# Kernel optimization log

Measured on AMD Instinct MI355X. Metric: run time of the kernel, lower is better.

Reference implementation:

```python
import jax, jax.numpy as jnp
import numpy as np

B, LQ, LKV = 2, 4096, 2048
DQ = DK = DV = 1024
H, DQK, DHV = 16, 64, 64
DOUT = 1024


def _band_mask(span, stride):
    # additive mask: 0 where 0 <= row - col*stride < span, else -inf
    rows = jnp.arange(LQ)[:, None]
    cols = jnp.arange(LKV)[None, :]
    s = rows - cols * stride
    valid = (s >= 0) & (s < span)
    return jnp.where(valid, 0.0, -jnp.inf).astype(jnp.float32)  # [LQ, LKV]


def setup_inputs() -> dict:
    key = jax.random.key(0)
    ks = jax.random.split(key, 7)
    return {
        "q": jax.random.normal(ks[0], (B, LQ, DQ), jnp.float32),
        "k": jax.random.normal(ks[1], (B, LKV, DK), jnp.float32),
        "v": jax.random.normal(ks[2], (B, LKV, DV), jnp.float32),
        # Linear weights stored as [in, out] (x @ W == torch Linear with W.T)
        "Wq": jax.random.normal(ks[3], (DQ, H * DQK), jnp.float32) / np.sqrt(DQ).astype(np.float32),
        "Wk": jax.random.normal(ks[4], (DK, H * DQK), jnp.float32) / np.sqrt(DK).astype(np.float32),
        "Wv": jax.random.normal(ks[5], (DV, H * DHV), jnp.float32) / np.sqrt(DV).astype(np.float32),
        "Wo": jax.random.normal(ks[6], (H * DHV, DOUT), jnp.float32) / np.sqrt(H * DHV).astype(np.float32),
        "span": 16,
        "stride": 2,
    }


def reference(q, k, v, Wq, Wk, Wv, Wo, span, stride):
    mask = _band_mask(span, stride)  # [LQ, LKV]
    Q = (q @ Wq).reshape(B, LQ, H, DQK)   # [B, LQ, H, DQK]
    K = (k @ Wk).reshape(B, LKV, H, DQK)  # [B, LKV, H, DQK]
    V = (v @ Wv).reshape(B, LKV, H, DHV)  # [B, LKV, H, DHV]
    scores = jnp.einsum("bqhd,bkhd->bhqk", Q, K) + mask  # [B, H, LQ, LKV]
    # NOTE: original code softmaxes over dim 2 == the QUERY axis (faithful)
    attn = jax.nn.softmax(scores, axis=2)
    ctx = jnp.einsum("bhqk,bkhd->bqhd", attn, V).reshape(B, LQ, H * DHV)
    return ctx @ Wo  # [B, LQ, DOUT]
```

## Files before the change

### kernel.cpp

```cpp
#include <hip/hip_runtime.h>
#include <cstdint>
#include <cstddef>


typedef _Float16 f16;
typedef _Float16 f16x8 __attribute__((ext_vector_type(8)));
typedef float v4f __attribute__((ext_vector_type(4)));

#define B_  2
#define LQ_ 4096
#define LKV_ 2048
#define DMODEL 1024
#define NH 16
#define HD 64
#define SPAN 16
#define STRIDE 2

#define NQ_ELEMS  ((size_t)B_ * LQ_ * DMODEL)
#define NKV_ELEMS ((size_t)B_ * LKV_ * DMODEL)

__device__ __forceinline__ void async_copy16(const f16* g, f16* l) {
    __builtin_amdgcn_global_load_lds((const __attribute__((address_space(1))) void*)g,
                                     (__attribute__((address_space(3))) void*)l, 16, 0, 0);
}

__global__ __launch_bounds__(256)
void prep_all(const float* __restrict__ W0, const float* __restrict__ W1,
              const float* __restrict__ W2, const float* __restrict__ W3,
              f16* __restrict__ T0, f16* __restrict__ T1,
              f16* __restrict__ T2, f16* __restrict__ T3,
              const float* __restrict__ q, const float* __restrict__ k,
              const float* __restrict__ v,
              f16* __restrict__ qh, f16* __restrict__ kh, f16* __restrict__ vh) {
    const int t = threadIdx.x;
    const int bid = blockIdx.x;
    if (bid < 1024) {
        const int z = bid >> 8, rem = bid & 255;
        const int bx = rem & 15, byy = rem >> 4;
        const float* W;
        f16* Wt;
        switch (z) {
            case 0: W = W0; Wt = T0; break;
            case 1: W = W1; Wt = T1; break;
            case 2: W = W2; Wt = T2; break;
            default: W = W3; Wt = T3; break;
        }
        __shared__ float tile[64][65];
        const int r0 = byy * 64, c0 = bx * 64;
        const int tx = t & 63, ty = t >> 6;
        for (int i = ty; i < 64; i += 4)
            tile[i][tx] = W[(long)(r0 + i) * DMODEL + c0 + tx];
        __syncthreads();
        for (int i = ty; i < 64; i += 4)
            Wt[(long)(c0 + i) * DMODEL + r0 + tx] = (f16)tile[tx][i];
    } else {
        const int cid = bid - 1024;
        const float* src;
        f16* dst;
        size_t base;
        if (cid < 4096)      { src = q; dst = qh; base = (size_t)cid * 2048; }
        else if (cid < 6144) { src = k; dst = kh; base = (size_t)(cid - 4096) * 2048; }
        else                 { src = v; dst = vh; base = (size_t)(cid - 6144) * 2048; }
        const size_t i = base + (size_t)t * 8;
        const float4 lo = *(const float4*)(src + i);
        const float4 hi = *(const float4*)(src + i + 4);
        f16x8 o = {(f16)lo.x, (f16)lo.y, (f16)lo.z, (f16)lo.w,
                   (f16)hi.x, (f16)hi.y, (f16)hi.z, (f16)hi.w};
        *(f16x8*)(dst + i) = o;
    }
}

template <bool OUT_F32>
__device__ __forceinline__ void gemm_body(const f16* __restrict__ Ah,
                                          const f16* __restrict__ Bt,
                                          void* __restrict__ Cv,
                                          int rowTile, int colTile) {
    constexpr int K = DMODEL, N = DMODEL;
    __shared__ f16 As[128 * 64];
    __shared__ f16 Bs[128 * 64];
    const int t = threadIdx.x;
    const int lane = t & 63;
    const int w = t >> 6;
    const int wm = w >> 1, wn = w & 1;
    const long rowBase = (long)rowTile * 128;
    const long colBase = (long)colTile * 128;
    const int qrow = lane & 15;
    const int quad = lane >> 4;

    v4f acc[4][4] = {};

    const int srow = t >> 3;
    const int schunk = t & 7;
    const int gchunk = schunk ^ (srow & 7);
    const f16* aptr = Ah + (rowBase + srow) * (long)K + gchunk * 8;
    const f16* bptr = Bt + (colBase + srow) * (long)K + gchunk * 8;
    f16* lA = &As[srow * 64 + schunk * 8];
    f16* lB = &Bs[srow * 64 + schunk * 8];

    for (int k0 = 0; k0 < K; k0 += 64) {
#pragma unroll
        for (int i = 0; i < 4; ++i)
            async_copy16(bptr + k0 + i * 32 * (long)K, lB + i * 2048);
#pragma unroll
        for (int i = 0; i < 4; ++i)
            async_copy16(aptr + k0 + i * 32 * (long)K, lA + i * 2048);
        __syncthreads();
#pragma unroll
        for (int s = 0; s < 2; ++s) {
            const int xk = (s * 4 + quad) ^ (qrow & 7);
            f16x8 af[4], bf[4];
#pragma unroll
            for (int mt = 0; mt < 4; ++mt)
                af[mt] = *(const f16x8*)(&As[(wm * 64 + mt * 16 + qrow) * 64 + xk * 8]);
#pragma unroll
            for (int nt = 0; nt < 4; ++nt)
                bf[nt] = *(const f16x8*)(&Bs[(wn * 64 + nt * 16 + qrow) * 64 + xk * 8]);
#pragma unroll
            for (int mt = 0; mt < 4; ++mt)
#pragma unroll
                for (int nt = 0; nt < 4; ++nt)
                    acc[mt][nt] = __builtin_amdgcn_mfma_f32_16x16x32_f16(
                        af[mt], bf[nt], acc[mt][nt], 0, 0, 0);
        }
        __syncthreads();
    }

#pragma unroll
    for (int mt = 0; mt < 4; ++mt)
#pragma unroll
        for (int nt = 0; nt < 4; ++nt) {
            const long col = colBase + wn * 64 + nt * 16 + qrow;
#pragma unroll
            for (int r = 0; r < 4; ++r) {
                const long row = rowBase + wm * 64 + mt * 16 + quad * 4 + r;
                if (OUT_F32)
                    ((float*)Cv)[row * (long)N + col] = acc[mt][nt][r];
                else
                    ((f16*)Cv)[row * (long)N + col] = (f16)acc[mt][nt][r];
            }
        }
}

__global__ __launch_bounds__(256, 2)
void gemm_qkv(const f16* __restrict__ A0, const f16* __restrict__ A1,
              const f16* __restrict__ A2, const f16* __restrict__ B0,
              const f16* __restrict__ B1, const f16* __restrict__ B2,
              f16* __restrict__ C0, f16* __restrict__ C1, f16* __restrict__ C2) {
    const int id = blockIdx.x;
    const int xcd = id & 7;
    const int g = id >> 3;
    const int ct = g & 7;
    int rowIdx = (g >> 3) + xcd * 16;
    const f16* A;
    const f16* Bt;
    f16* C;
    if (rowIdx < 64) {
        A = A0; Bt = B0; C = C0;
    } else if (rowIdx < 96) {
        A = A1; Bt = B1; C = C1; rowIdx -= 64;
    } else {
        A = A2; Bt = B2; C = C2; rowIdx -= 96;
    }
    gemm_body<false>(A, Bt, (void*)C, rowIdx, ct);
}

__global__ __launch_bounds__(256, 2)
void gemm_out(const f16* __restrict__ A, const f16* __restrict__ Bt,
              float* __restrict__ C) {
    const int id = blockIdx.x;
    const int xcd = id & 7;
    const int g = id >> 3;
    const int ct = g & 7;
    const int rowIdx = (g >> 3) + xcd * 8;
    gemm_body<true>(A, Bt, (void*)C, rowIdx, ct);
}

__global__ __launch_bounds__(256)
void attn_scores(const f16* __restrict__ Q, const f16* __restrict__ Km,
                 float* __restrict__ attnw) {
    const int c0 = blockIdx.x * 4, b = blockIdx.y;
    const int t = threadIdx.x;
    __shared__ f16 Qs[24 * 1032];
    __shared__ f16 Ks[4 * 1032];

#pragma unroll
    for (int it = 0; it < 12; ++it) {
        const int ch = t + 256 * it;
        const int row = ch >> 7, off = (ch & 127) * 8;
        int qq = 2 * c0 + row;
        if (qq > LQ_ - 1) qq = LQ_ - 1;
        f16x8 x = *(const f16x8*)(Q + (size_t)(b * LQ_ + qq) * DMODEL + off);
        const int h = off >> 6, bb = (off >> 3) & 7;
        *(f16x8*)(&Qs[row * 1032 + h * 64 + ((bb + h) & 7) * 8]) = x;
    }
#pragma unroll
    for (int it = 0; it < 2; ++it) {
        const int ch = t + 256 * it;
        const int row = ch >> 7, off = (ch & 127) * 8;
        f16x8 x = *(const f16x8*)(Km + (size_t)(b * LKV_ + c0 + row) * DMODEL + off);
        const int h = off >> 6, bb = (off >> 3) & 7;
        *(f16x8*)(&Ks[row * 1032 + h * 64 + ((bb + h) & 7) * 8]) = x;
    }
    __syncthreads();

    const int h = t >> 4, j = t & 15;
#pragma unroll
    for (int ci = 0; ci < 4; ++ci) {
        const int c = c0 + ci;
        const int q = STRIDE * c + j;
        const int row = 2 * ci + j;
        float a = 0.f;
#pragma unroll
        for (int bb = 0; bb < 8; ++bb) {
            const int off = h * 64 + ((bb + h) & 7) * 8;
            f16x8 qv = *(const f16x8*)(&Qs[row * 1032 + off]);
            f16x8 kv = *(const f16x8*)(&Ks[ci * 1032 + off]);
#pragma unroll
            for (int u = 0; u < 8; ++u) a += (float)qv[u] * (float)kv[u];
        }
        float s = (q < LQ_) ? a : -1e30f;
        float m = s;
#pragma unroll
        for (int o = 1; o < 16; o <<= 1) m = fmaxf(m, __shfl_xor(m, o, 64));
        float p = (q < LQ_) ? __expf(s - m) : 0.f;
        float sum = p;
#pragma unroll
        for (int o = 1; o < 16; o <<= 1) sum += __shfl_xor(sum, o, 64);
        attnw[(size_t)((b * LKV_ + c) * NH + h) * SPAN + j] = p / sum;
    }
}

__global__ __launch_bounds__(256)
void ctx_gather(const float* __restrict__ attnw, const f16* __restrict__ V,
                f16* __restrict__ ctx) {
    const int q0 = blockIdx.x * 16, b = blockIdx.y;
    const int t = threadIdx.x;
    const int kbase = (q0 >> 1) - 7;
    __shared__ f16 Vs[16 * 1024];
    __shared__ float A_lds[16 * 256];

#pragma unroll
    for (int it = 0; it < 8; ++it) {
        const int ch = t + 256 * it;
        const int row = ch >> 7, off = (ch & 127) * 8;
        int k = kbase + row;
        k = (k < 0) ? 0 : ((k > LKV_ - 1) ? LKV_ - 1 : k);
        *(f16x8*)(&Vs[row * 1024 + off]) =
            *(const f16x8*)(V + (size_t)(b * LKV_ + k) * DMODEL + off);
    }
#pragma unroll
    for (int it = 0; it < 4; ++it) {
        const int ch = t + 256 * it;
        const int row = ch >> 6, off = (ch & 63) * 4;
        int k = kbase + row;
        k = (k < 0) ? 0 : ((k > LKV_ - 1) ? LKV_ - 1 : k);
        *(float4*)(&A_lds[row * 256 + off]) =
            *(const float4*)(attnw + (size_t)(b * LKV_ + k) * 256 + off);
    }
    __syncthreads();

    const int chunk = t & 127;
    const int h = chunk >> 3;
    const int d8 = (chunk & 7) * 8;
    const int qh = t >> 7;
    const int aoff = h * 16 + qh;
    const int kq0 = q0 >> 1;

#pragma unroll
    for (int qp = 0; qp < 8; ++qp) {
        const int q = q0 + qp * 2 + qh;
        float acc[8] = {0.f, 0.f, 0.f, 0.f, 0.f, 0.f, 0.f, 0.f};
#pragma unroll
        for (int i = 0; i < 8; ++i) {
            if (kq0 + qp - i < 0) break;
            const int rr = 7 + qp - i;
            const float wgt = A_lds[rr * 256 + aoff + 2 * i];
            const f16x8 v8 = *(const f16x8*)(&Vs[rr * 1024 + h * 64 + d8]);
#pragma unroll
            for (int u = 0; u < 8; ++u) acc[u] += wgt * (float)v8[u];
        }
        f16x8 o = {(f16)acc[0], (f16)acc[1], (f16)acc[2], (f16)acc[3],
                   (f16)acc[4], (f16)acc[5], (f16)acc[6], (f16)acc[7]};
        *(f16x8*)(ctx + (size_t)(b * LQ_ + q) * DMODEL + h * HD + d8) = o;
    }
}

extern "C" void kernel_launch(void* const* d_in, const int* in_sizes, int n_in,
                              void* d_out, int out_size, void* d_ws, size_t ws_size,
                              hipStream_t stream) {
    const float* q  = (const float*)d_in[0];
    const float* k  = (const float*)d_in[1];
    const float* v  = (const float*)d_in[2];
    const float* Wq = (const float*)d_in[3];
    const float* Wk = (const float*)d_in[4];
    const float* Wv = (const float*)d_in[5];
    const float* Wo = (const float*)d_in[6];
    float* out = (float*)d_out;

    const size_t NW = (size_t)DMODEL * DMODEL;

    char* p = (char*)d_ws;
    f16* WqT = (f16*)p; p += NW * 2;
    f16* WkT = (f16*)p; p += NW * 2;
    f16* WvT = (f16*)p; p += NW * 2;
    f16* WoT = (f16*)p; p += NW * 2;
    f16* Qh  = (f16*)p; p += NQ_ELEMS * 2;
    f16* Kh  = (f16*)p; p += NKV_ELEMS * 2;
    f16* Vh  = (f16*)p; p += NKV_ELEMS * 2;
    f16* qf  = (f16*)p; p += NQ_ELEMS * 2;
    f16* kf  = (f16*)p; p += NKV_ELEMS * 2;
    f16* vf  = (f16*)p; p += NKV_ELEMS * 2;
    f16* ctxh = qf;
    float* attnw = (float*)kf;

    prep_all<<<dim3(9216), 256, 0, stream>>>(Wq, Wk, Wv, Wo, WqT, WkT, WvT, WoT,
                                             q, k, v, qf, kf, vf);

    gemm_qkv<<<dim3(1024), 256, 0, stream>>>(qf, kf, vf, WqT, WkT, WvT,
                                             Qh, Kh, Vh);

    attn_scores<<<dim3(LKV_ / 4, B_), 256, 0, stream>>>(Qh, Kh, attnw);

    ctx_gather<<<dim3(LQ_ / 16, B_), 256, 0, stream>>>(attnw, Vh, ctxh);

    gemm_out<<<dim3(512), 256, 0, stream>>>(ctxh, WoT, out);
}
```

Before: 213.8 us.

## Rewrite QKV projection GEMM with 256x256 tiles and fine-grained pipelined LDS staging

Replaces the 128x128, 256-thread QKV GEMM with a 256x256-tile, 512-thread kernel. It uses XOR-swizzled LDS, double-buffered async global-to-LDS copies interleaved with quarter-tile MFMA phases, explicit waitcnt and barrier scheduling, and priority boosts around the MFMA blocks. The goal is more data reuse per loaded tile and better overlap of memory with compute. The trade-off is a grid of only 256 blocks on a 256-CU part, roughly one wave of blocks, and large LDS and register use that may limit occupancy and make the hand-placed waitcnt counts fragile.

```diff
diff --git a/kernel.cpp b/kernel.cpp
--- a/kernel.cpp
+++ b/kernel.cpp
@@ -18,6 +18,13 @@
 
 #define NQ_ELEMS  ((size_t)B_ * LQ_ * DMODEL)
 #define NKV_ELEMS ((size_t)B_ * LKV_ * DMODEL)
+
+#define BAR()   __builtin_amdgcn_s_barrier()
+#define LGKM0() asm volatile("s_waitcnt lgkmcnt(0)" ::: "memory")
+#define SB0()   __builtin_amdgcn_sched_barrier(0)
+#define VM4()   asm volatile("s_waitcnt vmcnt(4)" ::: "memory")
+#define VM2()   asm volatile("s_waitcnt vmcnt(2)" ::: "memory")
+#define VM0()   asm volatile("s_waitcnt vmcnt(0)" ::: "memory")
 
 __device__ __forceinline__ void async_copy16(const f16* g, f16* l) {
     __builtin_amdgcn_global_load_lds((const __attribute__((address_space(1))) void*)g,
@@ -70,6 +77,128 @@
     }
 }
 
+__device__ __forceinline__ void gemm_qkv_body(const f16* __restrict__ Ah,
+                                              const f16* __restrict__ Bt,
+                                              f16* __restrict__ C,
+                                              int rowTile, int colTile) {
+    constexpr int K = DMODEL, N = DMODEL, NT = K / 64;
+    __shared__ f16 lds[2 * 32768];
+
+    const int t = threadIdx.x;
+    const int lane = t & 63, w = t >> 6;
+    const int wm = w >> 2, wn = w & 3;
+    const int qrow = lane & 15, quad = lane >> 4;
+    const long rowBase = (long)rowTile * 256;
+    const long colBase = (long)colTile * 256;
+
+    const int srow = t >> 3, sch = t & 7;
+    const int gch = sch ^ (srow & 7);
+    const f16* aBase = Ah + (rowBase + srow) * (long)K + gch * 8;
+    const f16* bBase = Bt + (colBase + srow) * (long)K + gch * 8;
+
+    v4f acc[8][4] = {};
+    f16x8 afr[4][2];
+    f16x8 bfr[4][2];
+
+    auto STAGE = [&](int tt2, int op, int half) {
+        f16* dst = &lds[(tt2 & 1) * 32768 + op * 16384 + half * 8192 + t * 8];
+        const f16* src = (op ? bBase : aBase) + (long)half * 128 * K + tt2 * 64;
+        async_copy16(src, dst);
+        async_copy16(src + 64 * (long)K, dst + 4096);
+    };
+    auto DSA = [&](int tt2, int h) {
+        const f16* lp = &lds[(tt2 & 1) * 32768];
+#pragma unroll
+        for (int m4 = 0; m4 < 4; ++m4)
+#pragma unroll
+            for (int s = 0; s < 2; ++s)
+                afr[m4][s] = *(const f16x8*)(lp +
+                    (h * 128 + wm * 64 + m4 * 16 + qrow) * 64 +
+                    (((s * 4 + quad) ^ (qrow & 7)) * 8));
+    };
+    auto DSB = [&](int tt2, int h) {
+        const f16* lp = &lds[(tt2 & 1) * 32768 + 16384];
+#pragma unroll
+        for (int n2 = 0; n2 < 2; ++n2)
+#pragma unroll
+            for (int s = 0; s < 2; ++s)
+                bfr[h * 2 + n2][s] = *(const f16x8*)(lp +
+                    (h * 128 + wn * 32 + n2 * 16 + qrow) * 64 +
+                    (((s * 4 + quad) ^ (qrow & 7)) * 8));
+    };
+    auto MQ = [&](int ah, int bh) {
+        __builtin_amdgcn_s_setprio(1);
+#pragma unroll
+        for (int s = 0; s < 2; ++s)
+#pragma unroll
+            for (int m4 = 0; m4 < 4; ++m4)
+#pragma unroll
+                for (int n2 = 0; n2 < 2; ++n2)
+                    acc[ah * 4 + m4][bh * 2 + n2] =
+                        __builtin_amdgcn_mfma_f32_16x16x32_f16(
+                            afr[m4][s], bfr[bh * 2 + n2][s],
+                            acc[ah * 4 + m4][bh * 2 + n2], 0, 0, 0);
+        __builtin_amdgcn_s_setprio(0);
+    };
+
+    STAGE(0, 0, 0); STAGE(0, 1, 0); STAGE(0, 1, 1); STAGE(0, 0, 1);
+    VM0();
+    BAR();
+
+#pragma unroll 2
+    for (int tt = 0; tt < NT; ++tt) {
+        const bool st = (tt + 1 < NT);
+        DSA(tt, 0); DSB(tt, 0);
+        if (st) STAGE(tt + 1, 0, 0);
+        BAR(); LGKM0(); SB0();
+        MQ(0, 0);
+        if (st) { VM4(); } else { VM2(); }
+        BAR();
+        DSB(tt, 1);
+        if (st) STAGE(tt + 1, 1, 0);
+        BAR(); LGKM0(); SB0();
+        MQ(0, 1);
+        if (st) { VM4(); } else { VM0(); }
+        BAR();
+        DSA(tt, 1);
+        if (st) STAGE(tt + 1, 1, 1);
+        BAR(); LGKM0(); SB0();
+        MQ(1, 0);
+        BAR();
+        if (st) STAGE(tt + 1, 0, 1);
+        MQ(1, 1);
+        if (st) VM4();
+        BAR();
+    }
+
+#pragma unroll
+    for (int m = 0; m < 8; ++m)
+#pragma unroll
+        for (int n = 0; n < 4; ++n) {
+            const int ah = m >> 2, m4 = m & 3;
+            const int bh = n >> 1, n2 = n & 1;
+            const long col = colBase + bh * 128 + wn * 32 + n2 * 16 + qrow;
+#pragma unroll
+            for (int r = 0; r < 4; ++r) {
+                const long row = rowBase + ah * 128 + wm * 64 + m4 * 16 + quad * 4 + r;
+                C[row * (long)N + col] = (f16)acc[m][n][r];
+            }
+        }
+}
+
+__global__ __launch_bounds__(512)
+void gemm_qkv(const f16* __restrict__ qf, const f16* __restrict__ kf,
+              const f16* __restrict__ vf, const f16* __restrict__ WqT,
+              const f16* __restrict__ WkT, const f16* __restrict__ WvT,
+              f16* __restrict__ Qh, f16* __restrict__ Kh, f16* __restrict__ Vh) {
+    const int id = (blockIdx.x & 7) * 32 + (blockIdx.x >> 3);
+    const f16* A; const f16* Bt; f16* C; int rt, ct;
+    if (id < 128)      { A = qf; Bt = WqT; C = Qh; rt = id >> 2; ct = id & 3; }
+    else if (id < 192) { const int g = id - 128; A = kf; Bt = WkT; C = Kh; rt = g >> 2; ct = g & 3; }
+    else               { const int g = id - 192; A = vf; Bt = WvT; C = Vh; rt = g >> 2; ct = g & 3; }
+    gemm_qkv_body(A, Bt, C, rt, ct);
+}
+
 template <bool OUT_F32>
 __device__ __forceinline__ void gemm_body(const f16* __restrict__ Ah,
                                           const f16* __restrict__ Bt,
@@ -142,29 +271,6 @@
 }
 
 __global__ __launch_bounds__(256, 2)
-void gemm_qkv(const f16* __restrict__ A0, const f16* __restrict__ A1,
-              const f16* __restrict__ A2, const f16* __restrict__ B0,
-              const f16* __restrict__ B1, const f16* __restrict__ B2,
-              f16* __restrict__ C0, f16* __restrict__ C1, f16* __restrict__ C2) {
-    const int id = blockIdx.x;
-    const int xcd = id & 7;
-    const int g = id >> 3;
-    const int ct = g & 7;
-    int rowIdx = (g >> 3) + xcd * 16;
-    const f16* A;
-    const f16* Bt;
-    f16* C;
-    if (rowIdx < 64) {
-        A = A0; Bt = B0; C = C0;
-    } else if (rowIdx < 96) {
-        A = A1; Bt = B1; C = C1; rowIdx -= 64;
-    } else {
-        A = A2; Bt = B2; C = C2; rowIdx -= 96;
-    }
-    gemm_body<false>(A, Bt, (void*)C, rowIdx, ct);
-}
-
-__global__ __launch_bounds__(256, 2)
 void gemm_out(const f16* __restrict__ A, const f16* __restrict__ Bt,
               float* __restrict__ C) {
     const int id = blockIdx.x;
@@ -316,8 +422,8 @@
     prep_all<<<dim3(9216), 256, 0, stream>>>(Wq, Wk, Wv, Wo, WqT, WkT, WvT, WoT,
                                              q, k, v, qf, kf, vf);
 
-    gemm_qkv<<<dim3(1024), 256, 0, stream>>>(qf, kf, vf, WqT, WkT, WvT,
-                                             Qh, Kh, Vh);
+    gemm_qkv<<<dim3(256), 512, 0, stream>>>(qf, kf, vf, WqT, WkT, WvT,
+                                            Qh, Kh, Vh);
 
     attn_scores<<<dim3(LKV_ / 4, B_), 256, 0, stream>>>(Qh, Kh, attnw);
 
```

Result: faster. 209.1 us (-2.2%).
